# Performance work log

Measured on AMD Instinct MI355X. Metric: run time of the kernel, lower is better.

The kernel has to match this reference:

```python
import jax, jax.numpy as jnp
import numpy as np

N_NODES = 50000
N_EDGES = 800000
IN_CH = 128
OUT_CH = 64
HEADS = 1
NEG_SLOPE = 0.2

def _glorot(key, shape):
    stdv = np.sqrt(6.0 / (shape[-2] + shape[-1]))
    return jax.random.uniform(key, shape, jnp.float32, -stdv, stdv)

def setup_inputs() -> dict:
    key = jax.random.key(0)
    k1, k2, k3, k4, k5 = jax.random.split(key, 5)
    x = jax.random.normal(k1, (N_NODES, IN_CH), jnp.float32)
    src = jax.random.randint(k2, (N_EDGES,), 0, N_NODES)
    dst = jax.random.randint(k3, (N_EDGES,), 0, N_NODES)
    # ensure no pre-existing self loops (remove_self_loops is then identity)
    dst = jnp.where(src == dst, (dst + 1) % N_NODES, dst)
    edge_index = jnp.stack([src, dst]).astype(jnp.int64)
    weight = _glorot(k4, (IN_CH, HEADS * OUT_CH))
    att = _glorot(k5, (1, HEADS, 2 * OUT_CH))
    bias = jnp.zeros((OUT_CH,), jnp.float32)
    return {"x": x, "edge_index": edge_index, "weight": weight, "att": att, "bias": bias}

def reference(x, edge_index, weight, att, bias):
    N = x.shape[0]
    # linear projection -> [N, heads, out]
    h = (x @ weight).reshape(N, HEADS, OUT_CH)
    # add self loops (input guaranteed free of self loops)
    loops = jnp.arange(N, dtype=edge_index.dtype)
    src = jnp.concatenate([edge_index[0], loops])  # source j
    dst = jnp.concatenate([edge_index[1], loops])  # target i
    x_j = h[src]   # [E+N, heads, out]
    x_i = h[dst]
    # attention logits: (cat([x_i, x_j]) * att).sum(-1) -> [E+N, heads]
    alpha = jnp.concatenate([x_i, x_j], axis=-1)
    alpha = (alpha * att).sum(axis=-1)
    alpha = jax.nn.leaky_relu(alpha, NEG_SLOPE)
    # segment softmax over destination nodes
    amax = jax.ops.segment_max(alpha, dst, num_segments=N)
    e = jnp.exp(alpha - amax[dst])
    esum = jax.ops.segment_sum(e, dst, num_segments=N)
    alpha = e / (esum[dst] + 1e-16)
    # message + scatter-add aggregation
    msg = x_j * alpha[:, :, None]
    out = jax.ops.segment_sum(msg, dst, num_segments=N)  # [N, heads, out]
    out = out.mean(axis=1) + bias
    # F.normalize (L2, dim=1, eps=1e-12); dropout is eval-mode identity
    norm = jnp.maximum(jnp.linalg.norm(out, axis=1, keepdims=True), 1e-12)
    return out / norm
```

## Files before the change

kernel.cpp:

```cpp
#include <hip/hip_runtime.h>
#include <math.h>

#define IN_CH 128
#define OUT_CH 64
#define NEG_SLOPE 0.2f
#define CAP 64

__device__ __forceinline__ unsigned short f2bf(float f) {
    unsigned u = __float_as_uint(f);
    unsigned r = (u + 0x7FFFu + ((u >> 16) & 1u)) >> 16;
    return (unsigned short)r;
}

__device__ __forceinline__ bool sniff_is64(const void* edges) {
    const unsigned* up = (const unsigned*)edges;
    bool is64 = true;
#pragma unroll
    for (int k = 0; k < 16; k++) is64 = is64 && (up[2 * k + 1] == 0u);
    return is64;
}

__global__ __launch_bounds__(256) void k_mm_cs(
        const float* __restrict__ x, const float* __restrict__ W,
        const float* __restrict__ att, unsigned short* __restrict__ h16,
        float* __restrict__ asrc, float* __restrict__ adst, int N,
        const void* __restrict__ edges, int* __restrict__ counts,
        int* __restrict__ slots, int* __restrict__ oflow_cnt,
        int2* __restrict__ oflow, int E, int mmb, int csb) {
    __shared__ float Ws[IN_CH * OUT_CH];
    int t = threadIdx.x;
    int bid = blockIdx.x;
    int lo = min(mmb, csb), M2 = 2 * lo;
    int role, id;
    if (bid < M2) { role = bid & 1; id = bid >> 1; }
    else          { role = (mmb > csb) ? 0 : 1; id = bid - M2 + lo; }

    if (role == 1) {
        int e0 = (id * 256 + t) * 4;
        if (e0 >= E) return;
        int s[4], d[4];
        bool full = (e0 + 3 < E);
        if (full) {
            if (sniff_is64(edges)) {
                const long long* p = (const long long*)edges;
#pragma unroll
                for (int i = 0; i < 4; i++) {
                    s[i] = (int)__builtin_nontemporal_load(p + e0 + i);
                    d[i] = (int)__builtin_nontemporal_load(p + (size_t)E + e0 + i);
                }
            } else {
                const int* p = (const int*)edges;
#pragma unroll
                for (int i = 0; i < 4; i++) {
                    s[i] = __builtin_nontemporal_load(p + e0 + i);
                    d[i] = __builtin_nontemporal_load(p + E + e0 + i);
                }
            }
#pragma unroll
            for (int i = 0; i < 4; i++) {
                int r = atomicAdd(counts + d[i], 1);
                if (r < CAP) {
                    slots[((size_t)d[i] << 6) + r] = s[i];
                } else {
                    int p2 = atomicAdd(oflow_cnt, 1);
                    oflow[p2] = make_int2(s[i], d[i]);
                }
            }
        } else {
            bool is64 = sniff_is64(edges);
            for (int i = 0; i < 4; i++) {
                if (e0 + i >= E) break;
                int sv, dv;
                if (is64) {
                    const long long* p = (const long long*)edges;
                    sv = (int)p[e0 + i];
                    dv = (int)p[(size_t)E + e0 + i];
                } else {
                    const int* p = (const int*)edges;
                    sv = p[e0 + i];
                    dv = p[E + e0 + i];
                }
                int r = atomicAdd(counts + dv, 1);
                if (r < CAP) {
                    slots[((size_t)dv << 6) + r] = sv;
                } else {
                    int p2 = atomicAdd(oflow_cnt, 1);
                    oflow[p2] = make_int2(sv, dv);
                }
            }
        }
        return;
    }

    for (int i = t * 4; i < IN_CH * OUT_CH; i += 256 * 4)
        *(float4*)&Ws[i] = *(const float4*)&W[i];
    int cg = t & 15, g = t >> 4;
    float4 att_d = *(const float4*)&att[cg * 4];
    float4 att_s = *(const float4*)&att[64 + cg * 4];
    __syncthreads();

    int n0 = id * 64 + g * 4;
    int nn[4];
#pragma unroll
    for (int m = 0; m < 4; m++) nn[m] = min(n0 + m, N - 1);

    float4 acc[4];
#pragma unroll
    for (int m = 0; m < 4; m++) acc[m] = make_float4(0.f, 0.f, 0.f, 0.f);

#pragma unroll 2
    for (int k4 = 0; k4 < IN_CH / 4; k4++) {
        float4 xv[4];
#pragma unroll
        for (int m = 0; m < 4; m++)
            xv[m] = *(const float4*)&x[(size_t)nn[m] * IN_CH + k4 * 4];
        float4 wv[4];
#pragma unroll
        for (int j = 0; j < 4; j++)
            wv[j] = *(const float4*)&Ws[(k4 * 4 + j) * OUT_CH + cg * 4];
#pragma unroll
        for (int m = 0; m < 4; m++) {
            acc[m].x = fmaf(xv[m].x, wv[0].x, acc[m].x);
            acc[m].y = fmaf(xv[m].x, wv[0].y, acc[m].y);
            acc[m].z = fmaf(xv[m].x, wv[0].z, acc[m].z);
            acc[m].w = fmaf(xv[m].x, wv[0].w, acc[m].w);
            acc[m].x = fmaf(xv[m].y, wv[1].x, acc[m].x);
            acc[m].y = fmaf(xv[m].y, wv[1].y, acc[m].y);
            acc[m].z = fmaf(xv[m].y, wv[1].z, acc[m].z);
            acc[m].w = fmaf(xv[m].y, wv[1].w, acc[m].w);
            acc[m].x = fmaf(xv[m].z, wv[2].x, acc[m].x);
            acc[m].y = fmaf(xv[m].z, wv[2].y, acc[m].y);
            acc[m].z = fmaf(xv[m].z, wv[2].z, acc[m].z);
            acc[m].w = fmaf(xv[m].z, wv[2].w, acc[m].w);
            acc[m].x = fmaf(xv[m].w, wv[3].x, acc[m].x);
            acc[m].y = fmaf(xv[m].w, wv[3].y, acc[m].y);
            acc[m].z = fmaf(xv[m].w, wv[3].z, acc[m].z);
            acc[m].w = fmaf(xv[m].w, wv[3].w, acc[m].w);
        }
    }

#pragma unroll
    for (int m = 0; m < 4; m++) {
        int node = n0 + m;
        if (node < N) {
            ushort4 hv;
            hv.x = f2bf(acc[m].x);
            hv.y = f2bf(acc[m].y);
            hv.z = f2bf(acc[m].z);
            hv.w = f2bf(acc[m].w);
            *(ushort4*)&h16[(size_t)node * OUT_CH + cg * 4] = hv;
        }
        float pd = acc[m].x * att_d.x + acc[m].y * att_d.y +
                   acc[m].z * att_d.z + acc[m].w * att_d.w;
        float ps = acc[m].x * att_s.x + acc[m].y * att_s.y +
                   acc[m].z * att_s.z + acc[m].w * att_s.w;
#pragma unroll
        for (int msk = 1; msk < 16; msk <<= 1) {
            pd += __shfl_xor(pd, msk, 64);
            ps += __shfl_xor(ps, msk, 64);
        }
        if (cg == 0 && node < N) { adst[node] = pd; asrc[node] = ps; }
    }
}

__global__ __launch_bounds__(256) void k_agg(const unsigned short* __restrict__ h16,
                                             const int* __restrict__ slots,
                                             const int* __restrict__ counts,
                                             const int* __restrict__ oflow_cnt,
                                             const int2* __restrict__ oflow,
                                             const float* __restrict__ asrc,
                                             const float* __restrict__ adst,
                                             const float* __restrict__ bias,
                                             float* __restrict__ out, int N) {
    __shared__ float2 stage[4][64];
    int lane = threadIdx.x & 63;
    int wid = threadIdx.x >> 6;
    int node = blockIdx.x * 4 + wid;
    if (node >= N) return;
    int half = lane >> 5;
    int ch2 = (lane & 31) * 2;

    float aD = adst[node];
    float a = aD + asrc[node];
    a = a > 0.f ? a : NEG_SLOPE * a;
    float w_self = __expf(a);
    unsigned hv = *(const unsigned*)&h16[(size_t)node * OUT_CH + ch2];
    float wse = half ? 0.f : w_self;
    float accx = wse * __uint_as_float(hv << 16);
    float accy = wse * __uint_as_float(hv & 0xFFFF0000u);

    int c = counts[node];
    int cs = min(c, CAP);
    int sv = 0;
    float wv = 0.f;
    if (lane < cs) {
        sv = slots[((size_t)node << 6) + lane];
        float av = aD + asrc[sv];
        av = av > 0.f ? av : NEG_SLOPE * av;
        wv = __expf(av);
    }
    float esum_lane = wv;
    stage[wid][lane] = make_float2(__int_as_float(sv), wv);

    for (int j = 0; j < cs; j += 16) {
#pragma unroll
        for (int k = 0; k < 8; k++) {
            float2 p = stage[wid][j + 2 * k + half];
            int s = __float_as_int(p.x);
            unsigned v = *(const unsigned*)&h16[((size_t)s << 6) + ch2];
            accx = fmaf(p.y, __uint_as_float(v << 16), accx);
            accy = fmaf(p.y, __uint_as_float(v & 0xFFFF0000u), accy);
        }
    }
    accx += __shfl_xor(accx, 32, 64);
    accy += __shfl_xor(accy, 32, 64);
#pragma unroll
    for (int m = 32; m >= 1; m >>= 1) esum_lane += __shfl_xor(esum_lane, m, 64);
    float esum = esum_lane + w_self;

    int oc = *oflow_cnt;
    if (oc > 0) {
        for (int i = 0; i < oc; i++) {
            int2 e = oflow[i];
            if (e.y == node) {
                float av = aD + asrc[e.x];
                av = av > 0.f ? av : NEG_SLOPE * av;
                float w = __expf(av);
                esum += w;
                unsigned v = *(const unsigned*)&h16[((size_t)e.x << 6) + ch2];
                accx = fmaf(w, __uint_as_float(v << 16), accx);
                accy = fmaf(w, __uint_as_float(v & 0xFFFF0000u), accy);
            }
        }
    }

    float inv = 1.f / (esum + 1e-16f);
    float2 bv = *(const float2*)&bias[ch2];
    float vx = accx * inv + bv.x;
    float vy = accy * inv + bv.y;
    float ss = vx * vx + vy * vy;
#pragma unroll
    for (int m = 16; m >= 1; m >>= 1) ss += __shfl_xor(ss, m, 64);
    float rinv = 1.f / fmaxf(sqrtf(ss), 1e-12f);
    if (!half)
        *(float2*)&out[(size_t)node * OUT_CH + ch2] = make_float2(vx * rinv, vy * rinv);
}

extern "C" void kernel_launch(void* const* d_in, const int* in_sizes, int n_in,
                              void* d_out, int out_size, void* d_ws, size_t ws_size,
                              hipStream_t stream) {
    const float* x    = (const float*)d_in[0];
    const void*  edges = d_in[1];
    const float* W    = (const float*)d_in[2];
    const float* att  = (const float*)d_in[3];
    const float* bias = (const float*)d_in[4];
    float* out = (float*)d_out;

    const int N = in_sizes[0] / IN_CH;
    const int E = in_sizes[1] / 2;
    const int MMB = (N + 63) / 64;
    const int CSB = (E + 1023) / 1024;

    char* ws = (char*)d_ws;
    size_t off = 0;
    auto alloc = [&](size_t bytes) -> void* {
        void* p = ws + off;
        off += bytes;
        off = (off + 255) & ~(size_t)255;
        return p;
    };
    int*            counts   = (int*)alloc((size_t)(N + 64) * 4);
    int*            slots    = (int*)alloc((size_t)N * CAP * 4);
    int2*           oflow    = (int2*)alloc((size_t)E * 8);
    unsigned short* h16      = (unsigned short*)alloc((size_t)N * OUT_CH * 2);
    float*          asrc     = (float*)alloc((size_t)N * 4);
    float*          adst     = (float*)alloc((size_t)N * 4);
    int*            oflow_cnt = counts + N;

    hipMemsetAsync(counts, 0, (size_t)(N + 64) * 4, stream);
    k_mm_cs<<<MMB + CSB, 256, 0, stream>>>(x, W, att, h16, asrc, adst, N,
                                           edges, counts, slots, oflow_cnt,
                                           oflow, E, MMB, CSB);
    k_agg<<<(N + 3) / 4, 256, 0, stream>>>(h16, slots, counts, oflow_cnt, oflow,
                                           asrc, adst, bias, out, N);
}
```

Baseline: 144.5 us.

## Shard edge bucketing by destination range per XCD with dynamic chunk queues

Each bucketing block reads its hardware XCC ID and handles only edges whose destination lies in that XCD's slice of the node range. The count atomics for a given node therefore stay within one XCD's L2 and use workgroup scope instead of device scope. Blocks pull 4096-edge chunks from a per-XCD atomic work queue and load indices with wide vector loads. Matmul blocks are spread evenly across the grid. The cost is that every XCD streams the whole edge list, about eight times the index traffic. It also relies on the XCC ID matching block placement and on workgroup-scope atomics staying correct across CUs within an XCD.

```diff
diff --git a/kernel.cpp b/kernel.cpp
--- a/kernel.cpp
+++ b/kernel.cpp
@@ -5,6 +5,10 @@
 #define OUT_CH 64
 #define NEG_SLOPE 0.2f
 #define CAP 64
+#define NSHARD 8
+#define CHUNK_EDGES 4096
+
+typedef long long ll2 __attribute__((ext_vector_type(2)));
 
 __device__ __forceinline__ unsigned short f2bf(float f) {
     unsigned u = __float_as_uint(f);
@@ -26,70 +30,101 @@
         float* __restrict__ asrc, float* __restrict__ adst, int N,
         const void* __restrict__ edges, int* __restrict__ counts,
         int* __restrict__ slots, int* __restrict__ oflow_cnt,
-        int2* __restrict__ oflow, int E, int mmb, int csb) {
+        int2* __restrict__ oflow, int E, int mmb, int nchunks,
+        int* __restrict__ queues) {
     __shared__ float Ws[IN_CH * OUT_CH];
     int t = threadIdx.x;
     int bid = blockIdx.x;
-    int lo = min(mmb, csb), M2 = 2 * lo;
-    int role, id;
-    if (bid < M2) { role = bid & 1; id = bid >> 1; }
-    else          { role = (mmb > csb) ? 0 : 1; id = bid - M2 + lo; }
-
-    if (role == 1) {
-        int e0 = (id * 256 + t) * 4;
-        if (e0 >= E) return;
-        int s[4], d[4];
-        bool full = (e0 + 3 < E);
-        if (full) {
-            if (sniff_is64(edges)) {
-                const long long* p = (const long long*)edges;
-#pragma unroll
-                for (int i = 0; i < 4; i++) {
-                    s[i] = (int)__builtin_nontemporal_load(p + e0 + i);
-                    d[i] = (int)__builtin_nontemporal_load(p + (size_t)E + e0 + i);
+    int total = gridDim.x;
+    int mbefore = (int)(((long long)bid * mmb) / total);
+    int mafter  = (int)(((long long)(bid + 1) * mmb) / total);
+    bool ismm = (mafter != mbefore);
+    int id = mbefore;
+
+    if (!ismm) {
+        int* chunk_sh = (int*)Ws;
+        int xcd;
+        asm volatile("s_getreg_b32 %0, hwreg(HW_REG_XCC_ID)" : "=s"(xcd));
+        xcd &= 7;
+        int lo = (int)(((long long)xcd * N) / NSHARD);
+        int hi = (int)(((long long)(xcd + 1) * N) / NSHARD);
+        bool is64 = sniff_is64(edges);
+        for (;;) {
+            if (t == 0)
+                *chunk_sh = __hip_atomic_fetch_add(queues + xcd * 16, 1,
+                                                   __ATOMIC_RELAXED,
+                                                   __HIP_MEMORY_SCOPE_WORKGROUP);
+            __syncthreads();
+            int chunk = *chunk_sh;
+            __syncthreads();
+            if (chunk >= nchunks) return;
+
+            int base = chunk * CHUNK_EDGES + t * 16;
+            int nv = E - base;
+            if (nv <= 0) continue;
+            if (nv > 16) nv = 16;
+            int dv[16], sv[16];
+            if (nv == 16) {
+                if (is64) {
+                    const ll2* pd = (const ll2*)((const long long*)edges +
+                                                 (size_t)E + base);
+                    const ll2* ps = (const ll2*)((const long long*)edges + base);
+#pragma unroll
+                    for (int i = 0; i < 8; i++) {
+                        ll2 w = pd[i];
+                        dv[2 * i] = (int)w.x; dv[2 * i + 1] = (int)w.y;
+                    }
+#pragma unroll
+                    for (int i = 0; i < 8; i++) {
+                        ll2 v = ps[i];
+                        sv[2 * i] = (int)v.x; sv[2 * i + 1] = (int)v.y;
+                    }
+                } else {
+                    const int4* pd = (const int4*)((const int*)edges + E + base);
+                    const int4* ps = (const int4*)((const int*)edges + base);
+#pragma unroll
+                    for (int i = 0; i < 4; i++) {
+                        int4 w = pd[i];
+                        dv[4 * i] = w.x; dv[4 * i + 1] = w.y;
+                        dv[4 * i + 2] = w.z; dv[4 * i + 3] = w.w;
+                    }
+#pragma unroll
+                    for (int i = 0; i < 4; i++) {
+                        int4 v = ps[i];
+                        sv[4 * i] = v.x; sv[4 * i + 1] = v.y;
+                        sv[4 * i + 2] = v.z; sv[4 * i + 3] = v.w;
+                    }
                 }
             } else {
-                const int* p = (const int*)edges;
-#pragma unroll
-                for (int i = 0; i < 4; i++) {
-                    s[i] = __builtin_nontemporal_load(p + e0 + i);
-                    d[i] = __builtin_nontemporal_load(p + E + e0 + i);
+                for (int i = 0; i < 16; i++) {
+                    if (i < nv) {
+                        if (is64) {
+                            dv[i] = (int)((const long long*)edges)[(size_t)E + base + i];
+                            sv[i] = (int)((const long long*)edges)[base + i];
+                        } else {
+                            dv[i] = ((const int*)edges)[E + base + i];
+                            sv[i] = ((const int*)edges)[base + i];
+                        }
+                    } else {
+                        dv[i] = -1; sv[i] = 0;
+                    }
                 }
             }
 #pragma unroll
-            for (int i = 0; i < 4; i++) {
-                int r = atomicAdd(counts + d[i], 1);
-                if (r < CAP) {
-                    slots[((size_t)d[i] << 6) + r] = s[i];
-                } else {
-                    int p2 = atomicAdd(oflow_cnt, 1);
-                    oflow[p2] = make_int2(s[i], d[i]);
+            for (int i = 0; i < 16; i++) {
+                int d = dv[i];
+                if (d >= lo && d < hi) {
+                    int r = __hip_atomic_fetch_add(counts + d, 1, __ATOMIC_RELAXED,
+                                                   __HIP_MEMORY_SCOPE_WORKGROUP);
+                    if (r < CAP) {
+                        slots[((size_t)d << 6) + r] = sv[i];
+                    } else {
+                        int p2 = atomicAdd(oflow_cnt, 1);
+                        oflow[p2] = make_int2(sv[i], d);
+                    }
                 }
             }
-        } else {
-            bool is64 = sniff_is64(edges);
-            for (int i = 0; i < 4; i++) {
-                if (e0 + i >= E) break;
-                int sv, dv;
-                if (is64) {
-                    const long long* p = (const long long*)edges;
-                    sv = (int)p[e0 + i];
-                    dv = (int)p[(size_t)E + e0 + i];
-                } else {
-                    const int* p = (const int*)edges;
-                    sv = p[e0 + i];
-                    dv = p[E + e0 + i];
-                }
-                int r = atomicAdd(counts + dv, 1);
-                if (r < CAP) {
-                    slots[((size_t)dv << 6) + r] = sv;
-                } else {
-                    int p2 = atomicAdd(oflow_cnt, 1);
-                    oflow[p2] = make_int2(sv, dv);
-                }
-            }
-        }
-        return;
+        }
     }
 
     for (int i = t * 4; i < IN_CH * OUT_CH; i += 256 * 4)
@@ -258,8 +293,10 @@
 
     const int N = in_sizes[0] / IN_CH;
     const int E = in_sizes[1] / 2;
+    const int NCHUNKS = (E + CHUNK_EDGES - 1) / CHUNK_EDGES;
     const int MMB = (N + 63) / 64;
-    const int CSB = (E + 1023) / 1024;
+    const int CSB = NSHARD * NCHUNKS;
+    const int grid = MMB + CSB;
 
     char* ws = (char*)d_ws;
     size_t off = 0;
@@ -269,18 +306,19 @@
         off = (off + 255) & ~(size_t)255;
         return p;
     };
-    int*            counts   = (int*)alloc((size_t)(N + 64) * 4);
+    int*            counts   = (int*)alloc((size_t)(N + 256) * 4);
     int*            slots    = (int*)alloc((size_t)N * CAP * 4);
     int2*           oflow    = (int2*)alloc((size_t)E * 8);
     unsigned short* h16      = (unsigned short*)alloc((size_t)N * OUT_CH * 2);
     float*          asrc     = (float*)alloc((size_t)N * 4);
     float*          adst     = (float*)alloc((size_t)N * 4);
     int*            oflow_cnt = counts + N;
-
-    hipMemsetAsync(counts, 0, (size_t)(N + 64) * 4, stream);
-    k_mm_cs<<<MMB + CSB, 256, 0, stream>>>(x, W, att, h16, asrc, adst, N,
-                                           edges, counts, slots, oflow_cnt,
-                                           oflow, E, MMB, CSB);
+    int*            queues    = counts + N + 64;
+
+    hipMemsetAsync(counts, 0, (size_t)(N + 256) * 4, stream);
+    k_mm_cs<<<grid, 256, 0, stream>>>(x, W, att, h16, asrc, adst, N,
+                                      edges, counts, slots, oflow_cnt,
+                                      oflow, E, MMB, NCHUNKS, queues);
     k_agg<<<(N + 3) / 4, 256, 0, stream>>>(h16, slots, counts, oflow_cnt, oflow,
                                            asrc, adst, bias, out, N);
 }
```

After: 160.5 us. 1.11x slower.
